# Performance work log

Measured on AMD Instinct MI355X. Metric: run time of the kernel, lower is better.

Reference implementation:

```python
import jax, jax.numpy as jnp
import numpy as np

H, P, G, NS, K = 8, 64, 64, 64, 3          # heads, dim_head, slice_num, d_state, d_conv
D_INNER = H * P                            # 512
CONV_DIM = D_INNER + 2 * NS                # 640
D_IN_PROJ = 2 * D_INNER + 2 * NS + 2 * H   # 1168


def setup_inputs() -> dict:
    key = jax.random.key(0)
    ks = jax.random.split(key, 10)
    dim, Bsz, N = 256, 4, 8192
    s = 0.02
    return {
        "x": jax.random.normal(ks[0], (Bsz, N, dim), jnp.float32),
        "W_fx": jax.random.normal(ks[1], (D_INNER, dim), jnp.float32) * s,
        "b_fx": jnp.zeros((D_INNER,), jnp.float32),
        "W_x": jax.random.normal(ks[2], (D_INNER, dim), jnp.float32) * s,
        "b_x": jnp.zeros((D_INNER,), jnp.float32),
        "W_slice": jax.random.normal(ks[3], (G, P), jnp.float32) * s,
        "b_slice": jnp.zeros((G,), jnp.float32),
        "temperature": jnp.full((1, H, 1, 1), 0.5, jnp.float32),
        "hy_in_w": jax.random.normal(ks[4], (D_IN_PROJ, D_INNER), jnp.float32) * s,
        "hy_conv_w": jax.random.normal(ks[5], (CONV_DIM, K), jnp.float32) * s,
        "hy_conv_b": jnp.zeros((CONV_DIM,), jnp.float32),
        "hy_dt_bias": jnp.log(jnp.expm1(jnp.full((H,), 0.01, jnp.float32))),
        "hy_A_log": jnp.log(jnp.linspace(1.0, 16.0, H)).astype(jnp.float32),
        "hy_D": jnp.ones((H,), jnp.float32),
        "hy_fcD_w": jax.random.normal(ks[6], (H, D_INNER), jnp.float32) * s,
        "hy_norm_w": jnp.ones((D_INNER,), jnp.float32),
        "hy_out_w": jax.random.normal(ks[7], (D_INNER, D_INNER), jnp.float32) * s,
        "out_w": jax.random.normal(ks[8], (dim, D_INNER), jnp.float32) * s,
        "out_b": jnp.zeros((dim,), jnp.float32),
    }


def _hydra(u, in_w, conv_w, conv_b, dt_bias, A_log, Dp, fcD_w, norm_w, out_w):
    # Bidirectional Mamba2-style selective scan (Hydra, non mem-eff path).
    Bt, L, _ = u.shape
    zxbcdt = u @ in_w.T                                   # (B, L, 1168)
    z = zxbcdt[..., :D_INNER]
    xBC = zxbcdt[..., D_INNER:D_INNER + CONV_DIM]
    dt = zxbcdt[..., -2 * H:]
    # fwd dts for fwd copies, time-flipped bwd dts stacked along batch
    dt = jnp.concatenate([dt[..., :H], jnp.flip(dt[..., H:], axis=1)], axis=0)
    dt = jax.nn.softplus(dt + dt_bias)                    # (2B, L, H)
    # depthwise causal conv, kernel K, left pad K-1 then silu
    xp = jnp.pad(xBC, ((0, 0), (K - 1, 0), (0, 0)))
    xBC = sum(xp[:, k:k + L, :] * conv_w[:, k] for k in range(K)) + conv_b
    xBC = jax.nn.silu(xBC)
    x = xBC[..., :D_INNER]
    Bm = xBC[..., D_INNER:D_INNER + NS]
    Cm = xBC[..., D_INNER + NS:]
    x_og = x
    x2 = jnp.concatenate([x, jnp.flip(x, 1)], 0).reshape(2 * Bt, L, H, P)
    B2 = jnp.concatenate([Bm, jnp.flip(Bm, 1)], 0)        # (2B, L, NS)
    C2 = jnp.concatenate([Cm, jnp.flip(Cm, 1)], 0)
    dA = jnp.exp(dt * (-jnp.exp(A_log)))                  # (2B, L, H)
    dBx = jnp.einsum('blh,bln,blhp->blhpn', dt, B2, x2)   # (2B, L, H, P, NS)

    def step(h, inp):
        dA_t, dBx_t, C_t = inp
        h = h * dA_t[:, :, None, None] + dBx_t
        return h, jnp.einsum('bhpn,bn->bhp', h, C_t)

    h0 = jnp.zeros((2 * Bt, H, P, NS), u.dtype)
    _, ys = jax.lax.scan(step, h0, (dA.transpose(1, 0, 2), dBx.transpose(1, 0, 2, 3, 4), C2.transpose(1, 0, 2)))
    y = ys.transpose(1, 0, 2, 3).reshape(2 * Bt, L, D_INNER)
    y_fw, y_bw = y[:Bt], jnp.flip(y[Bt:], 1)
    # quasiseparable: strictly-lower (shift fwd) + strictly-upper (shift bwd) + diagonal
    y = jnp.pad(y_fw[:, :-1], ((0, 0), (1, 0), (0, 0))) + jnp.pad(y_bw[:, 1:], ((0, 0), (0, 1), (0, 0)))
    y = y + x_og * jnp.repeat(x_og @ fcD_w.T + Dp, P, axis=-1)
    # gated RMSNorm (gate before norm), then out projection
    yg = y * jax.nn.silu(z)
    yg = yg * jax.lax.rsqrt(jnp.mean(jnp.square(yg), -1, keepdims=True) + 1e-5) * norm_w
    return yg @ out_w.T


def reference(x, W_fx, b_fx, W_x, b_x, W_slice, b_slice, temperature,
              hy_in_w, hy_conv_w, hy_conv_b, hy_dt_bias, hy_A_log, hy_D,
              hy_fcD_w, hy_norm_w, hy_out_w, out_w, out_b):
    B, N, _ = x.shape
    fx = (x @ W_fx.T + b_fx).reshape(B, N, H, P).transpose(0, 2, 1, 3)   # (B,H,N,P)
    xm = (x @ W_x.T + b_x).reshape(B, N, H, P).transpose(0, 2, 1, 3)
    temp = jnp.maximum(temperature, 1e-6)
    sw = jax.nn.softmax((xm @ W_slice.T + b_slice) / temp, axis=-1)      # (B,H,N,G)
    snorm = sw.sum(2)                                                     # (B,H,G)
    st = jnp.einsum('bhnc,bhng->bhgc', fx, sw) / (snorm + 1e-5)[..., None]
    st = st.transpose(0, 2, 1, 3).reshape(B, G, D_INNER)                  # (B,G,512)
    ot = _hydra(st, hy_in_w, hy_conv_w, hy_conv_b, hy_dt_bias, hy_A_log, hy_D,
                hy_fcD_w, hy_norm_w, hy_out_w)
    ot = ot.reshape(B, G, H, P).transpose(0, 2, 1, 3)                     # (B,H,G,P)
    out = jnp.einsum('bhgc,bhng->bhnc', ot, sw).transpose(0, 2, 1, 3).reshape(B, N, D_INNER)
    return out @ out_w.T + out_b
```

## Files before the change

kernel.cpp:

```cpp
#include <hip/hip_runtime.h>
#include <hip/hip_bf16.h>
#include <cstdint>
#include <cstddef>

#define Hh 8
#define DIN 512
#define CONVD 640
#define DPROJ 1168
#define NTOK 8192
#define DIM 256

typedef __attribute__((ext_vector_type(8))) short short8;
typedef __attribute__((ext_vector_type(4))) float f32x4;

static __device__ __forceinline__ float sigmoidf_(float x) { return 1.f / (1.f + expf(-x)); }
static __device__ __forceinline__ unsigned short f2b(float f) {
  __hip_bfloat16 h = __float2bfloat16(f);
  return *(unsigned short*)&h;
}
static __device__ __forceinline__ float b2f(unsigned short u) {
  union { unsigned int i; float f; } cv; cv.i = ((unsigned int)u) << 16; return cv.f;
}

__global__ __launch_bounds__(256) void k_cvt(
    const float* __restrict__ wfx, const float* __restrict__ wx, const float* __restrict__ outw,
    const float* __restrict__ inw, const float* __restrict__ how,
    const float* __restrict__ bfx, const float* __restrict__ bx,
    unsigned short* __restrict__ wcat, unsigned short* __restrict__ outwb,
    unsigned short* __restrict__ inwb, unsigned short* __restrict__ howb,
    float* __restrict__ bcat) {
  const int e = (blockIdx.x * 256 + threadIdx.x) * 4;
  if (e >= 1253376) {
    const int i = e - 1253376;
    float4 v;
    if (i < 512) v = *(const float4*)(bfx + i);
    else         v = *(const float4*)(bx + (i - 512));
    *(float4*)(bcat + i) = v;
    return;
  }
  const float* src; unsigned short* dst; int i;
  if (e < 131072)        { i = e;           src = wfx;  dst = wcat; }
  else if (e < 262144)   { i = e - 131072;  src = wx;   dst = wcat + 131072; }
  else if (e < 393216)   { i = e - 262144;  src = outw; dst = outwb; }
  else if (e < 991232)   { i = e - 393216;  src = inw;  dst = inwb; }
  else                   { i = e - 991232;  src = how;  dst = howb; }
  float4 v = *(const float4*)(src + i);
  ushort4 o;
  o.x = f2b(v.x); o.y = f2b(v.y); o.z = f2b(v.z); o.w = f2b(v.w);
  *(ushort4*)(dst + i) = o;
}

__global__ __launch_bounds__(256) void k_front(
    const float* __restrict__ x, const unsigned short* __restrict__ wcat,
    const float* __restrict__ bcat, const float* __restrict__ Wslice,
    const float* __restrict__ bslice, const float* __restrict__ temperature,
    unsigned short* __restrict__ cb, unsigned short* __restrict__ swb) {
  __shared__ unsigned short lds[17408];
  unsigned short* As = lds;
  unsigned short* Bs = lds + 8320;
  const int tid = threadIdx.x;
  const int m0 = blockIdx.x * 128;
  const int n0 = blockIdx.y * 128;
  const int w = tid >> 6, lane = tid & 63;
  const int l15 = lane & 15, kq = lane >> 4;
  const int wm = (w & 1) * 64, wn = (w >> 1) * 64;
  float bs[4];
#pragma unroll
  for (int j = 0; j < 4; ++j) bs[j] = bcat[n0 + wn + j * 16 + l15];
  f32x4 acc[4][4];
#pragma unroll
  for (int i = 0; i < 4; ++i)
#pragma unroll
    for (int j = 0; j < 4; ++j) acc[i][j] = (f32x4){0.f, 0.f, 0.f, 0.f};
  for (int kt = 0; kt < 256; kt += 64) {
#pragma unroll
    for (int i = 0; i < 4; ++i) {
      const int c = tid + 256 * i, m = c >> 3, kb = c & 7;
      const float* xs = &x[(size_t)(m0 + m) * 256 + kt + kb * 8];
      float4 v0 = *(const float4*)xs;
      float4 v1 = *(const float4*)(xs + 4);
      short8 av;
      av[0] = (short)f2b(v0.x); av[1] = (short)f2b(v0.y);
      av[2] = (short)f2b(v0.z); av[3] = (short)f2b(v0.w);
      av[4] = (short)f2b(v1.x); av[5] = (short)f2b(v1.y);
      av[6] = (short)f2b(v1.z); av[7] = (short)f2b(v1.w);
      *(short8*)&As[(kb * 130 + m) * 8] = av;
      *(short8*)&Bs[(kb * 130 + m) * 8] = *(const short8*)&wcat[(size_t)(n0 + m) * 256 + kt + kb * 8];
    }
    __syncthreads();
#pragma unroll
    for (int kw = 0; kw < 2; ++kw) {
      short8 af[4], bfr[4];
#pragma unroll
      for (int i = 0; i < 4; ++i) {
        af[i]  = *(const short8*)&As[((kw * 4 + kq) * 130 + wm + i * 16 + l15) * 8];
        bfr[i] = *(const short8*)&Bs[((kw * 4 + kq) * 130 + wn + i * 16 + l15) * 8];
      }
#pragma unroll
      for (int i = 0; i < 4; ++i)
#pragma unroll
        for (int j = 0; j < 4; ++j)
          acc[i][j] = __builtin_amdgcn_mfma_f32_16x16x32_bf16(af[i], bfr[j], acc[i][j], 0, 0, 0);
    }
    __syncthreads();
  }
  unsigned short* Cs = lds;
#pragma unroll
  for (int i = 0; i < 4; ++i)
#pragma unroll
    for (int j = 0; j < 4; ++j)
#pragma unroll
      for (int r = 0; r < 4; ++r) {
        const int m = wm + i * 16 + kq * 4 + r;
        const int n = wn + j * 16 + l15;
        Cs[m * 136 + n] = f2b(acc[i][j][r] + bs[j]);
      }
  __syncthreads();
  if (blockIdx.y < 4) {
#pragma unroll
    for (int it = 0; it < 8; ++it) {
      const int c = tid + 256 * it;
      const int m = c >> 4, seg = c & 15;
      *(short8*)&cb[(size_t)(m0 + m) * 512 + n0 + seg * 8] = *(const short8*)&Cs[m * 136 + seg * 8];
    }
    return;
  }
  const int h0 = (n0 - 512) >> 6;
  const int bidx = m0 >> 13, nb = m0 & (NTOK - 1);
  short8 sbfr[2][4];
#pragma unroll
  for (int kt = 0; kt < 2; ++kt)
#pragma unroll
    for (int j = 0; j < 4; ++j) {
      const float* wp = Wslice + (j * 16 + l15) * 64 + kt * 32 + kq * 8;
      short8 t;
#pragma unroll
      for (int u = 0; u < 8; ++u) t[u] = (short)f2b(wp[u]);
      sbfr[kt][j] = t;
    }
  float sbs[4];
#pragma unroll
  for (int j = 0; j < 4; ++j) sbs[j] = bslice[j * 16 + l15];
  f32x4 sacc[2][2][4];
#pragma unroll
  for (int hl = 0; hl < 2; ++hl)
#pragma unroll
    for (int i = 0; i < 2; ++i)
#pragma unroll
      for (int j = 0; j < 4; ++j) sacc[hl][i][j] = (f32x4){0.f, 0.f, 0.f, 0.f};
#pragma unroll
  for (int hl = 0; hl < 2; ++hl)
#pragma unroll
    for (int kt = 0; kt < 2; ++kt) {
      short8 af[2];
#pragma unroll
      for (int i = 0; i < 2; ++i)
        af[i] = *(const short8*)&Cs[(w * 32 + i * 16 + l15) * 136 + hl * 64 + kt * 32 + kq * 8];
#pragma unroll
      for (int i = 0; i < 2; ++i)
#pragma unroll
        for (int j = 0; j < 4; ++j)
          sacc[hl][i][j] = __builtin_amdgcn_mfma_f32_16x16x32_bf16(af[i], sbfr[kt][j], sacc[hl][i][j], 0, 0, 0);
    }
  __syncthreads();
#pragma unroll
  for (int hl = 0; hl < 2; ++hl) {
    const float invt = 1.f / fmaxf(temperature[h0 + hl], 1e-6f);
#pragma unroll
    for (int i = 0; i < 2; ++i)
#pragma unroll
      for (int r = 0; r < 4; ++r) {
        float v[4];
        float m = -1e30f;
#pragma unroll
        for (int j = 0; j < 4; ++j) { v[j] = (sacc[hl][i][j][r] + sbs[j]) * invt; m = fmaxf(m, v[j]); }
#pragma unroll
        for (int off = 8; off; off >>= 1) m = fmaxf(m, __shfl_xor(m, off));
        float s = 0.f;
#pragma unroll
        for (int j = 0; j < 4; ++j) { v[j] = expf(v[j] - m); s += v[j]; }
#pragma unroll
        for (int off = 8; off; off >>= 1) s += __shfl_xor(s, off);
        const float inv = 1.f / s;
        const int row = w * 32 + i * 16 + kq * 4 + r;
#pragma unroll
        for (int j = 0; j < 4; ++j) Cs[row * 136 + hl * 64 + j * 16 + l15] = f2b(v[j] * inv);
      }
  }
  __syncthreads();
#pragma unroll
  for (int it = 0; it < 8; ++it) {
    const int c = tid + 256 * it;
    const int head = c >> 10, row = (c >> 3) & 127, seg = c & 7;
    *(short8*)&swb[((size_t)(bidx * 8 + h0 + head) * NTOK + nb + row) * 64 + seg * 8] =
        *(const short8*)&Cs[row * 136 + head * 64 + seg * 8];
  }
}

__global__ __launch_bounds__(256) void k_st(
    const unsigned short* __restrict__ swb, const unsigned short* __restrict__ cb,
    float* __restrict__ st_raw, float* __restrict__ snorm) {
  __shared__ unsigned short swT[64][136];
  __shared__ unsigned short fxT[64][136];
  const int tid = threadIdx.x;
  const int bh = blockIdx.y;
  const int b = bh >> 3, h = bh & 7;
  const int nbase = blockIdx.x * 512;
  const int w = tid >> 6, lane = tid & 63;
  const int l15 = lane & 15, kq = lane >> 4;
  f32x4 acc[4];
#pragma unroll
  for (int i = 0; i < 4; ++i) acc[i] = (f32x4){0.f, 0.f, 0.f, 0.f};
  float sn = 0.f;
  for (int nc = 0; nc < 4; ++nc) {
    const int n0 = nbase + nc * 128;
#pragma unroll
    for (int i = 0; i < 4; ++i) {
      const int c = tid + 256 * i, n = c >> 3, gc = c & 7;
      short8 sv = *(const short8*)&swb[((size_t)bh * NTOK + n0 + n) * 64 + gc * 8];
      short8 fv = *(const short8*)&cb[((size_t)(b * NTOK) + n0 + n) * 512 + h * 64 + gc * 8];
#pragma unroll
      for (int u = 0; u < 8; ++u) {
        swT[gc * 8 + u][n] = (unsigned short)sv[u];
        fxT[gc * 8 + u][n] = (unsigned short)fv[u];
      }
    }
    __syncthreads();
    {
      const int g = tid & 63, q = tid >> 6;
#pragma unroll
      for (int nn = 0; nn < 32; ++nn) sn += b2f(swT[g][q * 32 + nn]);
    }
#pragma unroll
    for (int kw = 0; kw < 4; ++kw) {
      short8 bfr = *(const short8*)&fxT[w * 16 + l15][kw * 32 + kq * 8];
#pragma unroll
      for (int mi = 0; mi < 4; ++mi) {
        short8 af = *(const short8*)&swT[mi * 16 + l15][kw * 32 + kq * 8];
        acc[mi] = __builtin_amdgcn_mfma_f32_16x16x32_bf16(af, bfr, acc[mi], 0, 0, 0);
      }
    }
    __syncthreads();
  }
  float* stp = st_raw + (size_t)bh * 4096;
#pragma unroll
  for (int mi = 0; mi < 4; ++mi)
#pragma unroll
    for (int r = 0; r < 4; ++r)
      atomicAdd(&stp[(mi * 16 + kq * 4 + r) * 64 + w * 16 + l15], acc[mi][r]);
  atomicAdd(&snorm[bh * 64 + (tid & 63)], sn);
}

__global__ __launch_bounds__(256) void k_stnorm(
    const float* __restrict__ st_raw, const float* __restrict__ snorm,
    unsigned short* __restrict__ st2b) {
  const int idx = blockIdx.x * 256 + threadIdx.x;
  const int p = idx & 63, g = (idx >> 6) & 63, h = (idx >> 12) & 7, b = idx >> 15;
  const float v = st_raw[idx] / (snorm[(b * Hh + h) * 64 + g] + 1e-5f);
  st2b[(size_t)(b * 64 + g) * DIN + h * 64 + p] = f2b(v);
}

__global__ __launch_bounds__(256) void k_inproj(
    const unsigned short* __restrict__ st2b, const unsigned short* __restrict__ inwb,
    float* __restrict__ zx) {
  const int tid = threadIdx.x;
  const int m0 = blockIdx.x * 64;
  const int n0 = blockIdx.y * 64;
  const int w = tid >> 6, lane = tid & 63;
  const int l15 = lane & 15, kq = lane >> 4;
  f32x4 acc[4];
#pragma unroll
  for (int j = 0; j < 4; ++j) acc[j] = (f32x4){0.f, 0.f, 0.f, 0.f};
  const int arow = m0 + w * 16 + l15;
#pragma unroll
  for (int kc = 0; kc < 16; ++kc) {
    const short8 af = *(const short8*)&st2b[(size_t)arow * DIN + kc * 32 + kq * 8];
#pragma unroll
    for (int j = 0; j < 4; ++j) {
      int brow = n0 + j * 16 + l15;
      if (brow >= DPROJ) brow = 0;
      const short8 bfr = *(const short8*)&inwb[(size_t)brow * DIN + kc * 32 + kq * 8];
      acc[j] = __builtin_amdgcn_mfma_f32_16x16x32_bf16(af, bfr, acc[j], 0, 0, 0);
    }
  }
#pragma unroll
  for (int j = 0; j < 4; ++j)
#pragma unroll
    for (int r = 0; r < 4; ++r) {
      const int m = m0 + w * 16 + kq * 4 + r;
      const int c = n0 + j * 16 + l15;
      if (c < DPROJ) zx[(size_t)m * DPROJ + c] = acc[j][r];
    }
}

__global__ __launch_bounds__(256) void k_prep(
    const float* __restrict__ zx, const float* __restrict__ convw, const float* __restrict__ convb,
    const float* __restrict__ dtbias, const float* __restrict__ Alog,
    float* __restrict__ xbc, float* __restrict__ dt2, float* __restrict__ ldA2) {
  const int idx = blockIdx.x * 256 + threadIdx.x;
  const int NCONV = 4 * 64 * CONVD;
  if (idx < NCONV) {
    const int c = idx % CONVD;
    const int l = (idx / CONVD) & 63;
    const int b = idx / (CONVD * 64);
    float acc = convb[c];
#pragma unroll
    for (int k = 0; k < 3; ++k) {
      const int ls = l - 2 + k;
      if (ls >= 0) acc += zx[(size_t)(b * 64 + ls) * DPROJ + DIN + c] * convw[c * 3 + k];
    }
    xbc[idx] = acc * sigmoidf_(acc);
  } else if (idx < NCONV + 8 * 64 * 8) {
    const int j = idx - NCONV;
    const int h = j & 7, l = (j >> 3) & 63, bb = j >> 9;
    float raw;
    if (bb < 4) raw = zx[(size_t)(bb * 64 + l) * DPROJ + 1152 + h];
    else        raw = zx[(size_t)((bb - 4) * 64 + (63 - l)) * DPROJ + 1160 + h];
    const float d = raw + dtbias[h];
    const float sp = (d > 20.f) ? d : log1pf(expf(d));
    dt2[j] = sp;
    ldA2[j] = sp * -expf(Alog[h]);
  }
}

__global__ __launch_bounds__(256) void k_ssm(
    const float* __restrict__ xbc, const float* __restrict__ dt2, const float* __restrict__ ldA2,
    float* __restrict__ ys) {
  __shared__ unsigned short s_C[64][72];
  __shared__ unsigned short s_Bm[64][72];
  __shared__ unsigned short s_X[64][72];
  __shared__ unsigned short s_G[64][72];
  __shared__ float s_L[64];
  __shared__ float s_dt[64];
  const int blk = blockIdx.x;
  const int h = blk & 7, bb = blk >> 3;
  const int b = (bb < 4) ? bb : bb - 4;
  const bool rev = bb >= 4;
  const int tid = threadIdx.x;
  const int w = tid >> 6, lane = tid & 63;
  const int l15 = lane & 15, kq = lane >> 4;
  {
    const int l = tid >> 2, part = tid & 3;
    const int t = rev ? 63 - l : l;
    const float* src = xbc + (size_t)(b * 64 + l) * CONVD + DIN + part * 32;
#pragma unroll
    for (int u = 0; u < 32; u += 4) {
      float4 v = *(const float4*)(src + u);
      const int c = part * 32 + u;
      unsigned short* dst = (c < 64) ? &s_Bm[t][c] : &s_C[t][c - 64];
      dst[0] = f2b(v.x); dst[1] = f2b(v.y); dst[2] = f2b(v.z); dst[3] = f2b(v.w);
    }
    const float* xs = xbc + (size_t)(b * 64 + l) * CONVD + h * 64 + part * 16;
#pragma unroll
    for (int u = 0; u < 16; u += 4) {
      float4 v = *(const float4*)(xs + u);
      const int p = part * 16 + u;
      s_X[p + 0][t] = f2b(v.x); s_X[p + 1][t] = f2b(v.y);
      s_X[p + 2][t] = f2b(v.z); s_X[p + 3][t] = f2b(v.w);
    }
  }
  if (w == 0) {
    const float dtv = dt2[(bb * 64 + lane) * 8 + h];
    float ld = ldA2[(bb * 64 + lane) * 8 + h];
#pragma unroll
    for (int off = 1; off < 64; off <<= 1) {
      const float o = __shfl_up(ld, off);
      if (lane >= off) ld += o;
    }
    s_L[lane] = ld;
    s_dt[lane] = dtv;
  }
  __syncthreads();
  f32x4 accS[4];
#pragma unroll
  for (int i = 0; i < 4; ++i) accS[i] = (f32x4){0.f, 0.f, 0.f, 0.f};
#pragma unroll
  for (int kw = 0; kw < 2; ++kw) {
    const short8 bfr = *(const short8*)&s_Bm[w * 16 + l15][kw * 32 + kq * 8];
#pragma unroll
    for (int i = 0; i < 4; ++i) {
      const short8 af = *(const short8*)&s_C[i * 16 + l15][kw * 32 + kq * 8];
      accS[i] = __builtin_amdgcn_mfma_f32_16x16x32_bf16(af, bfr, accS[i], 0, 0, 0);
    }
  }
  const int s_idx = w * 16 + l15;
  const float Ls = s_L[s_idx];
  const float dts = s_dt[s_idx];
#pragma unroll
  for (int i = 0; i < 4; ++i)
#pragma unroll
    for (int r = 0; r < 4; ++r) {
      const int t = i * 16 + kq * 4 + r;
      const float g = (s_idx <= t) ? accS[i][r] * expf(s_L[t] - Ls) * dts : 0.f;
      s_G[t][s_idx] = f2b(g);
    }
  __syncthreads();
  f32x4 accY[4];
#pragma unroll
  for (int i = 0; i < 4; ++i) accY[i] = (f32x4){0.f, 0.f, 0.f, 0.f};
#pragma unroll
  for (int kw = 0; kw < 2; ++kw) {
    const short8 bfr = *(const short8*)&s_X[w * 16 + l15][kw * 32 + kq * 8];
#pragma unroll
    for (int i = 0; i < 4; ++i) {
      const short8 af = *(const short8*)&s_G[i * 16 + l15][kw * 32 + kq * 8];
      accY[i] = __builtin_amdgcn_mfma_f32_16x16x32_bf16(af, bfr, accY[i], 0, 0, 0);
    }
  }
#pragma unroll
  for (int i = 0; i < 4; ++i)
#pragma unroll
    for (int r = 0; r < 4; ++r) {
      const int t = i * 16 + kq * 4 + r;
      ys[(((size_t)(bb * 64 + t) * 8 + h) << 6) + w * 16 + l15] = accY[i][r];
    }
}

__global__ __launch_bounds__(256) void k_gate(
    const float* __restrict__ ys, const float* __restrict__ xbc, const float* __restrict__ zx,
    const float* __restrict__ fcdw, const float* __restrict__ Dp,
    const float* __restrict__ normw, unsigned short* __restrict__ ygb) {
  __shared__ float red[256][9];
  __shared__ float s_xfc[8];
  const int bl = blockIdx.x;
  const int b = bl >> 6, l = bl & 63;
  const int tid = threadIdx.x;
  const float xog0 = xbc[(size_t)bl * CONVD + tid];
  const float xog1 = xbc[(size_t)bl * CONVD + 256 + tid];
#pragma unroll
  for (int h = 0; h < 8; ++h)
    red[tid][h] = xog0 * fcdw[h * DIN + tid] + xog1 * fcdw[h * DIN + 256 + tid];
  __syncthreads();
  for (int s = 128; s > 0; s >>= 1) {
    if (tid < s) {
#pragma unroll
      for (int h = 0; h < 8; ++h) red[tid][h] += red[tid + s][h];
    }
    __syncthreads();
  }
  if (tid < 8) s_xfc[tid] = red[0][tid] + Dp[tid];
  __syncthreads();
  float ygv[2];
  float sumsq = 0.f;
#pragma unroll
  for (int ci = 0; ci < 2; ++ci) {
    const int c = tid + ci * 256;
    const int h = c >> 6, p = c & 63;
    float yv = 0.f;
    if (l >= 1)  yv += ys[(((size_t)(b * 64 + (l - 1)) * 8 + h) << 6) + p];
    if (l <= 62) yv += ys[(((size_t)((4 + b) * 64 + (62 - l)) * 8 + h) << 6) + p];
    const float xog = (ci == 0) ? xog0 : xog1;
    yv += xog * s_xfc[h];
    const float z = zx[(size_t)bl * DPROJ + c];
    const float g = yv * (z * sigmoidf_(z));
    ygv[ci] = g;
    sumsq += g * g;
  }
  red[tid][0] = sumsq;
  __syncthreads();
  for (int s = 128; s > 0; s >>= 1) {
    if (tid < s) red[tid][0] += red[tid + s][0];
    __syncthreads();
  }
  const float scale = 1.f / sqrtf(red[0][0] / 512.f + 1e-5f);
#pragma unroll
  for (int ci = 0; ci < 2; ++ci) {
    const int c = tid + ci * 256;
    ygb[(size_t)bl * DIN + c] = f2b(ygv[ci] * scale * normw[c]);
  }
}

__global__ __launch_bounds__(256) void k_oproj(
    const unsigned short* __restrict__ ygb, const unsigned short* __restrict__ howb,
    unsigned short* __restrict__ otT) {
  __shared__ unsigned short Cs[64][72];
  const int tid = threadIdx.x;
  const int b = blockIdx.x;
  const int h = blockIdx.y;
  const int m0 = b * 64, n0 = h * 64;
  const int w = tid >> 6, lane = tid & 63;
  const int l15 = lane & 15, kq = lane >> 4;
  f32x4 acc[4];
#pragma unroll
  for (int j = 0; j < 4; ++j) acc[j] = (f32x4){0.f, 0.f, 0.f, 0.f};
  const int arow = m0 + w * 16 + l15;
#pragma unroll
  for (int kc = 0; kc < 16; ++kc) {
    const short8 af = *(const short8*)&ygb[(size_t)arow * DIN + kc * 32 + kq * 8];
#pragma unroll
    for (int j = 0; j < 4; ++j) {
      const int brow = n0 + j * 16 + l15;
      const short8 bfr = *(const short8*)&howb[(size_t)brow * DIN + kc * 32 + kq * 8];
      acc[j] = __builtin_amdgcn_mfma_f32_16x16x32_bf16(af, bfr, acc[j], 0, 0, 0);
    }
  }
#pragma unroll
  for (int j = 0; j < 4; ++j)
#pragma unroll
    for (int r = 0; r < 4; ++r) {
      const int g = w * 16 + kq * 4 + r;
      const int p = j * 16 + l15;
      Cs[p][g] = f2b(acc[j][r]);
    }
  __syncthreads();
#pragma unroll
  for (int it = 0; it < 2; ++it) {
    const int c = tid + 256 * it;
    const int p = c >> 3, seg = c & 7;
    *(short8*)&otT[(((size_t)(b * 8 + h) * 64 + p) << 6) + seg * 8] = *(const short8*)&Cs[p][seg * 8];
  }
}

__global__ __launch_bounds__(256) void k_mixfinal(
    const unsigned short* __restrict__ swb, const unsigned short* __restrict__ otT,
    const unsigned short* __restrict__ outwb, const float* __restrict__ outb,
    float* __restrict__ out) {
  __shared__ unsigned short lm[33280];
  const int blk = blockIdx.x;
  const int b = blk >> 7;
  const int t0 = (blk & 127) * 64;
  const int tid = threadIdx.x;
  const int w = tid >> 6, lane = tid & 63;
  const int l15 = lane & 15, kq = lane >> 4;
#pragma unroll
  for (int hh = 0; hh < 2; ++hh) {
    const int h = w * 2 + hh;
    const int bh = b * 8 + h;
    f32x4 acc[4][4];
#pragma unroll
    for (int i = 0; i < 4; ++i)
#pragma unroll
      for (int j = 0; j < 4; ++j) acc[i][j] = (f32x4){0.f, 0.f, 0.f, 0.f};
#pragma unroll
    for (int kt = 0; kt < 2; ++kt) {
      short8 af[4], bfr[4];
#pragma unroll
      for (int i = 0; i < 4; ++i) {
        af[i]  = *(const short8*)&swb[((size_t)bh * NTOK + t0 + i * 16 + l15) * 64 + kt * 32 + kq * 8];
        bfr[i] = *(const short8*)&otT[(((size_t)bh * 64 + i * 16 + l15) << 6) + kt * 32 + kq * 8];
      }
#pragma unroll
      for (int i = 0; i < 4; ++i)
#pragma unroll
        for (int j = 0; j < 4; ++j)
          acc[i][j] = __builtin_amdgcn_mfma_f32_16x16x32_bf16(af[i], bfr[j], acc[i][j], 0, 0, 0);
    }
#pragma unroll
    for (int i = 0; i < 4; ++i)
#pragma unroll
      for (int j = 0; j < 4; ++j)
#pragma unroll
        for (int r = 0; r < 4; ++r)
          lm[(i * 16 + kq * 4 + r) * 520 + h * 64 + j * 16 + l15] = f2b(acc[i][j][r]);
  }
  __syncthreads();
  float ob[4];
#pragma unroll
  for (int j = 0; j < 4; ++j) ob[j] = outb[w * 64 + j * 16 + l15];
  f32x4 facc[4][4];
#pragma unroll
  for (int i = 0; i < 4; ++i)
#pragma unroll
    for (int j = 0; j < 4; ++j) facc[i][j] = (f32x4){0.f, 0.f, 0.f, 0.f};
#pragma unroll
  for (int kt = 0; kt < 16; ++kt) {
    short8 af[4], bfr[4];
#pragma unroll
    for (int i = 0; i < 4; ++i) {
      af[i]  = *(const short8*)&lm[(i * 16 + l15) * 520 + kt * 32 + kq * 8];
      bfr[i] = *(const short8*)&outwb[(size_t)(w * 64 + i * 16 + l15) * 512 + kt * 32 + kq * 8];
    }
#pragma unroll
    for (int i = 0; i < 4; ++i)
#pragma unroll
      for (int j = 0; j < 4; ++j)
        facc[i][j] = __builtin_amdgcn_mfma_f32_16x16x32_bf16(af[i], bfr[j], facc[i][j], 0, 0, 0);
  }
  __syncthreads();
  float* lf = (float*)lm;
#pragma unroll
  for (int i = 0; i < 4; ++i)
#pragma unroll
    for (int j = 0; j < 4; ++j)
#pragma unroll
      for (int r = 0; r < 4; ++r)
        lf[(i * 16 + kq * 4 + r) * 260 + w * 64 + j * 16 + l15] = facc[i][j][r] + ob[j];
  __syncthreads();
#pragma unroll
  for (int it = 0; it < 16; ++it) {
    const int c = tid + 256 * it;
    const int row = c >> 6, seg = c & 63;
    *(float4*)&out[((size_t)(b * NTOK + t0 + row)) * 256 + seg * 4] =
        *(const float4*)&lf[row * 260 + seg * 4];
  }
}

extern "C" void kernel_launch(void* const* d_in, const int* in_sizes, int n_in,
                              void* d_out, int out_size, void* d_ws, size_t ws_size,
                              hipStream_t stream) {
  const float* x      = (const float*)d_in[0];
  const float* Wfx    = (const float*)d_in[1];
  const float* bfx    = (const float*)d_in[2];
  const float* Wx     = (const float*)d_in[3];
  const float* bx     = (const float*)d_in[4];
  const float* Wslice = (const float*)d_in[5];
  const float* bslice = (const float*)d_in[6];
  const float* temp   = (const float*)d_in[7];
  const float* inw    = (const float*)d_in[8];
  const float* convw  = (const float*)d_in[9];
  const float* convb  = (const float*)d_in[10];
  const float* dtbias = (const float*)d_in[11];
  const float* Alog   = (const float*)d_in[12];
  const float* Dp     = (const float*)d_in[13];
  const float* fcdw   = (const float*)d_in[14];
  const float* normw  = (const float*)d_in[15];
  const float* how    = (const float*)d_in[16];
  const float* outw   = (const float*)d_in[17];
  const float* outb   = (const float*)d_in[18];

  unsigned short* us = (unsigned short*)d_ws;
  unsigned short* cb     = us;
  unsigned short* swb    = cb + 16777216;
  unsigned short* wcatb  = swb + 16777216;
  unsigned short* outwbf = wcatb + 262144;
  unsigned short* otTb   = outwbf + 131072;
  unsigned short* inwb   = otTb + 131072;
  unsigned short* howb   = inwb + 598016;
  unsigned short* st2b   = howb + 262144;
  unsigned short* ygbb   = st2b + 131072;
  float* fbase = (float*)(ygbb + 131072);
  float* bcat   = fbase;
  float* st_raw = bcat + 1024;
  float* snorm  = st_raw + 131072;
  float* zx     = snorm + 2048;
  float* xbc    = zx + 299008;
  float* dt2    = xbc + 163840;
  float* ldA2   = dt2 + 4096;
  float* ysb    = ldA2 + 4096;

  hipMemsetAsync(st_raw, 0, (131072 + 2048) * sizeof(float), stream);

  k_cvt     <<<dim3(1225),    256, 0, stream>>>(Wfx, Wx, outw, inw, how, bfx, bx,
                                                wcatb, outwbf, inwb, howb, bcat);
  k_front   <<<dim3(256, 8),  256, 0, stream>>>(x, wcatb, bcat, Wslice, bslice, temp, cb, swb);
  k_st      <<<dim3(16, 32),  256, 0, stream>>>(swb, cb, st_raw, snorm);
  k_stnorm  <<<dim3(512),     256, 0, stream>>>(st_raw, snorm, st2b);
  k_inproj  <<<dim3(4, 19),   256, 0, stream>>>(st2b, inwb, zx);
  k_prep    <<<dim3(656),     256, 0, stream>>>(zx, convw, convb, dtbias, Alog, xbc, dt2, ldA2);
  k_ssm     <<<dim3(64),      256, 0, stream>>>(xbc, dt2, ldA2, ysb);
  k_gate    <<<dim3(256),     256, 0, stream>>>(ysb, xbc, zx, fcdw, Dp, normw, ygbb);
  k_oproj   <<<dim3(4, 8),    256, 0, stream>>>(ygbb, howb, otTb);
  k_mixfinal<<<dim3(512),     256, 0, stream>>>(swb, otTb, outwbf, outb, (float*)d_out);
}
```

Baseline: 267.7 us.

## Emit transposed fx and slice-weight layouts from front GEMM, pre-convert x to bf16

The front GEMM now writes the fx projection and the softmax slice weights in a token-contiguous transposed layout (head*64+channel rows by token columns), alongside the existing slice-weight copy. The reduction kernel can then feed MFMA straight from global memory, with no LDS transpose and no barriers. The input x is converted to bf16 in a separate pre-pass inside the weight-convert kernel. In exchange it writes an extra full-size slice-weight copy and a bf16 copy of x, adding about 48 MB of global traffic, and k_front uses twice the shared memory.

```diff
diff --git a/kernel.cpp b/kernel.cpp
--- a/kernel.cpp
+++ b/kernel.cpp
@@ -23,15 +23,15 @@
 }
 
 __global__ __launch_bounds__(256) void k_cvt(
-    const float* __restrict__ wfx, const float* __restrict__ wx, const float* __restrict__ outw,
-    const float* __restrict__ inw, const float* __restrict__ how,
+    const float* __restrict__ x, const float* __restrict__ wfx, const float* __restrict__ wx,
+    const float* __restrict__ outw, const float* __restrict__ inw, const float* __restrict__ how,
     const float* __restrict__ bfx, const float* __restrict__ bx,
-    unsigned short* __restrict__ wcat, unsigned short* __restrict__ outwb,
-    unsigned short* __restrict__ inwb, unsigned short* __restrict__ howb,
-    float* __restrict__ bcat) {
+    unsigned short* __restrict__ xb, unsigned short* __restrict__ wcat,
+    unsigned short* __restrict__ outwb, unsigned short* __restrict__ inwb,
+    unsigned short* __restrict__ howb, float* __restrict__ bcat) {
   const int e = (blockIdx.x * 256 + threadIdx.x) * 4;
-  if (e >= 1253376) {
-    const int i = e - 1253376;
+  if (e >= 9641984) {
+    const int i = e - 9641984;
     float4 v;
     if (i < 512) v = *(const float4*)(bfx + i);
     else         v = *(const float4*)(bx + (i - 512));
@@ -39,11 +39,12 @@
     return;
   }
   const float* src; unsigned short* dst; int i;
-  if (e < 131072)        { i = e;           src = wfx;  dst = wcat; }
-  else if (e < 262144)   { i = e - 131072;  src = wx;   dst = wcat + 131072; }
-  else if (e < 393216)   { i = e - 262144;  src = outw; dst = outwb; }
-  else if (e < 991232)   { i = e - 393216;  src = inw;  dst = inwb; }
-  else                   { i = e - 991232;  src = how;  dst = howb; }
+  if (e < 8388608)       { i = e;           src = x;    dst = xb; }
+  else if (e < 8519680)  { i = e - 8388608; src = wfx;  dst = wcat; }
+  else if (e < 8650752)  { i = e - 8519680; src = wx;   dst = wcat + 131072; }
+  else if (e < 8781824)  { i = e - 8650752; src = outw; dst = outwb; }
+  else if (e < 9379840)  { i = e - 8781824; src = inw;  dst = inwb; }
+  else                   { i = e - 9379840; src = how;  dst = howb; }
   float4 v = *(const float4*)(src + i);
   ushort4 o;
   o.x = f2b(v.x); o.y = f2b(v.y); o.z = f2b(v.z); o.w = f2b(v.w);
@@ -51,11 +52,12 @@
 }
 
 __global__ __launch_bounds__(256) void k_front(
-    const float* __restrict__ x, const unsigned short* __restrict__ wcat,
+    const unsigned short* __restrict__ xb, const unsigned short* __restrict__ wcat,
     const float* __restrict__ bcat, const float* __restrict__ Wslice,
     const float* __restrict__ bslice, const float* __restrict__ temperature,
-    unsigned short* __restrict__ cb, unsigned short* __restrict__ swb) {
-  __shared__ unsigned short lds[17408];
+    unsigned short* __restrict__ cbT, unsigned short* __restrict__ swb,
+    unsigned short* __restrict__ swT) {
+  __shared__ unsigned short lds[34816];
   unsigned short* As = lds;
   unsigned short* Bs = lds + 8320;
   const int tid = threadIdx.x;
@@ -76,15 +78,7 @@
 #pragma unroll
     for (int i = 0; i < 4; ++i) {
       const int c = tid + 256 * i, m = c >> 3, kb = c & 7;
-      const float* xs = &x[(size_t)(m0 + m) * 256 + kt + kb * 8];
-      float4 v0 = *(const float4*)xs;
-      float4 v1 = *(const float4*)(xs + 4);
-      short8 av;
-      av[0] = (short)f2b(v0.x); av[1] = (short)f2b(v0.y);
-      av[2] = (short)f2b(v0.z); av[3] = (short)f2b(v0.w);
-      av[4] = (short)f2b(v1.x); av[5] = (short)f2b(v1.y);
-      av[6] = (short)f2b(v1.z); av[7] = (short)f2b(v1.w);
-      *(short8*)&As[(kb * 130 + m) * 8] = av;
+      *(short8*)&As[(kb * 130 + m) * 8] = *(const short8*)&xb[(size_t)(m0 + m) * 256 + kt + kb * 8];
       *(short8*)&Bs[(kb * 130 + m) * 8] = *(const short8*)&wcat[(size_t)(n0 + m) * 256 + kt + kb * 8];
     }
     __syncthreads();
@@ -104,7 +98,32 @@
     }
     __syncthreads();
   }
+  const int bidx = m0 >> 13, nb = m0 & (NTOK - 1);
+  if (blockIdx.y < 4) {
+    unsigned short* CsT = lds;
+#pragma unroll
+    for (int i = 0; i < 4; ++i)
+#pragma unroll
+      for (int j = 0; j < 4; ++j)
+#pragma unroll
+        for (int r = 0; r < 4; ++r) {
+          const int n = wm + i * 16 + kq * 4 + r;
+          const int pc = wn + j * 16 + l15;
+          CsT[pc * 136 + n] = f2b(acc[i][j][r] + bs[j]);
+        }
+    __syncthreads();
+    const int h0fx = blockIdx.y * 2;
+#pragma unroll
+    for (int it = 0; it < 8; ++it) {
+      const int c = tid + 256 * it;
+      const int pr = c >> 4, seg = c & 15;
+      const int row = (bidx * 8 + h0fx + (pr >> 6)) * 64 + (pr & 63);
+      *(short8*)&cbT[(size_t)row * NTOK + nb + seg * 8] = *(const short8*)&CsT[pr * 136 + seg * 8];
+    }
+    return;
+  }
   unsigned short* Cs = lds;
+  unsigned short* CsT2 = lds + 17408;
 #pragma unroll
   for (int i = 0; i < 4; ++i)
 #pragma unroll
@@ -116,17 +135,7 @@
         Cs[m * 136 + n] = f2b(acc[i][j][r] + bs[j]);
       }
   __syncthreads();
-  if (blockIdx.y < 4) {
-#pragma unroll
-    for (int it = 0; it < 8; ++it) {
-      const int c = tid + 256 * it;
-      const int m = c >> 4, seg = c & 15;
-      *(short8*)&cb[(size_t)(m0 + m) * 512 + n0 + seg * 8] = *(const short8*)&Cs[m * 136 + seg * 8];
-    }
-    return;
-  }
   const int h0 = (n0 - 512) >> 6;
-  const int bidx = m0 >> 13, nb = m0 & (NTOK - 1);
   short8 sbfr[2][4];
 #pragma unroll
   for (int kt = 0; kt < 2; ++kt)
@@ -184,7 +193,11 @@
         const float inv = 1.f / s;
         const int row = w * 32 + i * 16 + kq * 4 + r;
 #pragma unroll
-        for (int j = 0; j < 4; ++j) Cs[row * 136 + hl * 64 + j * 16 + l15] = f2b(v[j] * inv);
+        for (int j = 0; j < 4; ++j) {
+          const unsigned short sv = f2b(v[j] * inv);
+          Cs[row * 136 + hl * 64 + j * 16 + l15] = sv;
+          CsT2[(hl * 64 + j * 16 + l15) * 136 + row] = sv;
+        }
       }
   }
   __syncthreads();
@@ -195,52 +208,35 @@
     *(short8*)&swb[((size_t)(bidx * 8 + h0 + head) * NTOK + nb + row) * 64 + seg * 8] =
         *(const short8*)&Cs[row * 136 + head * 64 + seg * 8];
   }
+#pragma unroll
+  for (int it = 0; it < 8; ++it) {
+    const int c = tid + 256 * it;
+    const int gl = c >> 4, seg = c & 15;
+    const int grow = (bidx * 8 + h0 + (gl >> 6)) * 64 + (gl & 63);
+    *(short8*)&swT[(size_t)grow * NTOK + nb + seg * 8] = *(const short8*)&CsT2[gl * 136 + seg * 8];
+  }
 }
 
 __global__ __launch_bounds__(256) void k_st(
-    const unsigned short* __restrict__ swb, const unsigned short* __restrict__ cb,
+    const unsigned short* __restrict__ swT, const unsigned short* __restrict__ fxT,
     float* __restrict__ st_raw, float* __restrict__ snorm) {
-  __shared__ unsigned short swT[64][136];
-  __shared__ unsigned short fxT[64][136];
   const int tid = threadIdx.x;
   const int bh = blockIdx.y;
-  const int b = bh >> 3, h = bh & 7;
   const int nbase = blockIdx.x * 512;
   const int w = tid >> 6, lane = tid & 63;
   const int l15 = lane & 15, kq = lane >> 4;
   f32x4 acc[4];
 #pragma unroll
   for (int i = 0; i < 4; ++i) acc[i] = (f32x4){0.f, 0.f, 0.f, 0.f};
-  float sn = 0.f;
-  for (int nc = 0; nc < 4; ++nc) {
-    const int n0 = nbase + nc * 128;
-#pragma unroll
-    for (int i = 0; i < 4; ++i) {
-      const int c = tid + 256 * i, n = c >> 3, gc = c & 7;
-      short8 sv = *(const short8*)&swb[((size_t)bh * NTOK + n0 + n) * 64 + gc * 8];
-      short8 fv = *(const short8*)&cb[((size_t)(b * NTOK) + n0 + n) * 512 + h * 64 + gc * 8];
-#pragma unroll
-      for (int u = 0; u < 8; ++u) {
-        swT[gc * 8 + u][n] = (unsigned short)sv[u];
-        fxT[gc * 8 + u][n] = (unsigned short)fv[u];
-      }
-    }
-    __syncthreads();
-    {
-      const int g = tid & 63, q = tid >> 6;
-#pragma unroll
-      for (int nn = 0; nn < 32; ++nn) sn += b2f(swT[g][q * 32 + nn]);
-    }
-#pragma unroll
-    for (int kw = 0; kw < 4; ++kw) {
-      short8 bfr = *(const short8*)&fxT[w * 16 + l15][kw * 32 + kq * 8];
-#pragma unroll
-      for (int mi = 0; mi < 4; ++mi) {
-        short8 af = *(const short8*)&swT[mi * 16 + l15][kw * 32 + kq * 8];
-        acc[mi] = __builtin_amdgcn_mfma_f32_16x16x32_bf16(af, bfr, acc[mi], 0, 0, 0);
-      }
-    }
-    __syncthreads();
+#pragma unroll
+  for (int kc = 0; kc < 16; ++kc) {
+    const int noff = nbase + kc * 32 + kq * 8;
+    const short8 bfr = *(const short8*)&fxT[((size_t)bh * 64 + w * 16 + l15) * NTOK + noff];
+#pragma unroll
+    for (int mi = 0; mi < 4; ++mi) {
+      const short8 af = *(const short8*)&swT[((size_t)bh * 64 + mi * 16 + l15) * NTOK + noff];
+      acc[mi] = __builtin_amdgcn_mfma_f32_16x16x32_bf16(af, bfr, acc[mi], 0, 0, 0);
+    }
   }
   float* stp = st_raw + (size_t)bh * 4096;
 #pragma unroll
@@ -248,7 +244,18 @@
 #pragma unroll
     for (int r = 0; r < 4; ++r)
       atomicAdd(&stp[(mi * 16 + kq * 4 + r) * 64 + w * 16 + l15], acc[mi][r]);
-  atomicAdd(&snorm[bh * 64 + (tid & 63)], sn);
+  {
+    const int g = tid & 63, q = tid >> 6;
+    const unsigned short* sp = &swT[((size_t)bh * 64 + g) * NTOK + nbase + q * 128];
+    float sn = 0.f;
+#pragma unroll
+    for (int u = 0; u < 16; ++u) {
+      short8 sv = *(const short8*)&sp[u * 8];
+#pragma unroll
+      for (int e = 0; e < 8; ++e) sn += b2f((unsigned short)sv[e]);
+    }
+    atomicAdd(&snorm[bh * 64 + g], sn);
+  }
 }
 
 __global__ __launch_bounds__(256) void k_stnorm(
@@ -619,9 +626,11 @@
   const float* outb   = (const float*)d_in[18];
 
   unsigned short* us = (unsigned short*)d_ws;
-  unsigned short* cb     = us;
-  unsigned short* swb    = cb + 16777216;
-  unsigned short* wcatb  = swb + 16777216;
+  unsigned short* cbT    = us;
+  unsigned short* swb    = cbT + 16777216;
+  unsigned short* swTb   = swb + 16777216;
+  unsigned short* xbfb   = swTb + 16777216;
+  unsigned short* wcatb  = xbfb + 8388608;
   unsigned short* outwbf = wcatb + 262144;
   unsigned short* otTb   = outwbf + 131072;
   unsigned short* inwb   = otTb + 131072;
@@ -640,10 +649,11 @@
 
   hipMemsetAsync(st_raw, 0, (131072 + 2048) * sizeof(float), stream);
 
-  k_cvt     <<<dim3(1225),    256, 0, stream>>>(Wfx, Wx, outw, inw, how, bfx, bx,
-                                                wcatb, outwbf, inwb, howb, bcat);
-  k_front   <<<dim3(256, 8),  256, 0, stream>>>(x, wcatb, bcat, Wslice, bslice, temp, cb, swb);
-  k_st      <<<dim3(16, 32),  256, 0, stream>>>(swb, cb, st_raw, snorm);
+  k_cvt     <<<dim3(9417),    256, 0, stream>>>(x, Wfx, Wx, outw, inw, how, bfx, bx,
+                                                xbfb, wcatb, outwbf, inwb, howb, bcat);
+  k_front   <<<dim3(256, 8),  256, 0, stream>>>(xbfb, wcatb, bcat, Wslice, bslice, temp,
+                                                cbT, swb, swTb);
+  k_st      <<<dim3(16, 32),  256, 0, stream>>>(swTb, cbT, st_raw, snorm);
   k_stnorm  <<<dim3(512),     256, 0, stream>>>(st_raw, snorm, st2b);
   k_inproj  <<<dim3(4, 19),   256, 0, stream>>>(st2b, inwb, zx);
   k_prep    <<<dim3(656),     256, 0, stream>>>(zx, convw, convb, dtbias, Alog, xbc, dt2, ldA2);
```

Result: no change. 270.6 us (+1.1%).

## Pre-convert x to bf16 and fuse stnorm/prep into in-projection kernel

Applied to the files above, without the earlier changes.

Moves the fp32-to-bf16 conversion of x out of the front GEMM into the conversion kernel, so the GEMM loads bf16 directly, and adjusts the LDS padding stride. It also folds the st normalization into the in-projection A-load, and the conv/SiLU and dt softplus into the in-projection epilogue via a shared tile, which removes two launches and the zx round trip. zx now stores only the z part. The risk is the extra pass over x (write plus reread of a 16MB bf16 copy) in exchange for lighter GEMM loads.

```diff
diff --git a/kernel.cpp b/kernel.cpp
--- a/kernel.cpp
+++ b/kernel.cpp
@@ -23,15 +23,15 @@
 }
 
 __global__ __launch_bounds__(256) void k_cvt(
-    const float* __restrict__ wfx, const float* __restrict__ wx, const float* __restrict__ outw,
-    const float* __restrict__ inw, const float* __restrict__ how,
+    const float* __restrict__ x, const float* __restrict__ wfx, const float* __restrict__ wx,
+    const float* __restrict__ outw, const float* __restrict__ inw, const float* __restrict__ how,
     const float* __restrict__ bfx, const float* __restrict__ bx,
-    unsigned short* __restrict__ wcat, unsigned short* __restrict__ outwb,
-    unsigned short* __restrict__ inwb, unsigned short* __restrict__ howb,
-    float* __restrict__ bcat) {
+    unsigned short* __restrict__ xb, unsigned short* __restrict__ wcat,
+    unsigned short* __restrict__ outwb, unsigned short* __restrict__ inwb,
+    unsigned short* __restrict__ howb, float* __restrict__ bcat) {
   const int e = (blockIdx.x * 256 + threadIdx.x) * 4;
-  if (e >= 1253376) {
-    const int i = e - 1253376;
+  if (e >= 9641984) {
+    const int i = e - 9641984;
     float4 v;
     if (i < 512) v = *(const float4*)(bfx + i);
     else         v = *(const float4*)(bx + (i - 512));
@@ -39,11 +39,12 @@
     return;
   }
   const float* src; unsigned short* dst; int i;
-  if (e < 131072)        { i = e;           src = wfx;  dst = wcat; }
-  else if (e < 262144)   { i = e - 131072;  src = wx;   dst = wcat + 131072; }
-  else if (e < 393216)   { i = e - 262144;  src = outw; dst = outwb; }
-  else if (e < 991232)   { i = e - 393216;  src = inw;  dst = inwb; }
-  else                   { i = e - 991232;  src = how;  dst = howb; }
+  if (e < 8388608)       { i = e;           src = x;    dst = xb; }
+  else if (e < 8519680)  { i = e - 8388608; src = wfx;  dst = wcat; }
+  else if (e < 8650752)  { i = e - 8519680; src = wx;   dst = wcat + 131072; }
+  else if (e < 8781824)  { i = e - 8650752; src = outw; dst = outwb; }
+  else if (e < 9379840)  { i = e - 8781824; src = inw;  dst = inwb; }
+  else                   { i = e - 9379840; src = how;  dst = howb; }
   float4 v = *(const float4*)(src + i);
   ushort4 o;
   o.x = f2b(v.x); o.y = f2b(v.y); o.z = f2b(v.z); o.w = f2b(v.w);
@@ -51,13 +52,13 @@
 }
 
 __global__ __launch_bounds__(256) void k_front(
-    const float* __restrict__ x, const unsigned short* __restrict__ wcat,
+    const unsigned short* __restrict__ xb, const unsigned short* __restrict__ wcat,
     const float* __restrict__ bcat, const float* __restrict__ Wslice,
     const float* __restrict__ bslice, const float* __restrict__ temperature,
     unsigned short* __restrict__ cb, unsigned short* __restrict__ swb) {
   __shared__ unsigned short lds[17408];
   unsigned short* As = lds;
-  unsigned short* Bs = lds + 8320;
+  unsigned short* Bs = lds + 8384;
   const int tid = threadIdx.x;
   const int m0 = blockIdx.x * 128;
   const int n0 = blockIdx.y * 128;
@@ -76,16 +77,8 @@
 #pragma unroll
     for (int i = 0; i < 4; ++i) {
       const int c = tid + 256 * i, m = c >> 3, kb = c & 7;
-      const float* xs = &x[(size_t)(m0 + m) * 256 + kt + kb * 8];
-      float4 v0 = *(const float4*)xs;
-      float4 v1 = *(const float4*)(xs + 4);
-      short8 av;
-      av[0] = (short)f2b(v0.x); av[1] = (short)f2b(v0.y);
-      av[2] = (short)f2b(v0.z); av[3] = (short)f2b(v0.w);
-      av[4] = (short)f2b(v1.x); av[5] = (short)f2b(v1.y);
-      av[6] = (short)f2b(v1.z); av[7] = (short)f2b(v1.w);
-      *(short8*)&As[(kb * 130 + m) * 8] = av;
-      *(short8*)&Bs[(kb * 130 + m) * 8] = *(const short8*)&wcat[(size_t)(n0 + m) * 256 + kt + kb * 8];
+      *(short8*)&As[(kb * 131 + m) * 8] = *(const short8*)&xb[(size_t)(m0 + m) * 256 + kt + kb * 8];
+      *(short8*)&Bs[(kb * 131 + m) * 8] = *(const short8*)&wcat[(size_t)(n0 + m) * 256 + kt + kb * 8];
     }
     __syncthreads();
 #pragma unroll
@@ -93,8 +86,8 @@
       short8 af[4], bfr[4];
 #pragma unroll
       for (int i = 0; i < 4; ++i) {
-        af[i]  = *(const short8*)&As[((kw * 4 + kq) * 130 + wm + i * 16 + l15) * 8];
-        bfr[i] = *(const short8*)&Bs[((kw * 4 + kq) * 130 + wn + i * 16 + l15) * 8];
+        af[i]  = *(const short8*)&As[((kw * 4 + kq) * 131 + wm + i * 16 + l15) * 8];
+        bfr[i] = *(const short8*)&Bs[((kw * 4 + kq) * 131 + wn + i * 16 + l15) * 8];
       }
 #pragma unroll
       for (int i = 0; i < 4; ++i)
@@ -116,6 +109,7 @@
         Cs[m * 136 + n] = f2b(acc[i][j][r] + bs[j]);
       }
   __syncthreads();
+  const int bidx = m0 >> 13, nb = m0 & (NTOK - 1);
   if (blockIdx.y < 4) {
 #pragma unroll
     for (int it = 0; it < 8; ++it) {
@@ -126,7 +120,6 @@
     return;
   }
   const int h0 = (n0 - 512) >> 6;
-  const int bidx = m0 >> 13, nb = m0 & (NTOK - 1);
   short8 sbfr[2][4];
 #pragma unroll
   for (int kt = 0; kt < 2; ++kt)
@@ -251,30 +244,33 @@
   atomicAdd(&snorm[bh * 64 + (tid & 63)], sn);
 }
 
-__global__ __launch_bounds__(256) void k_stnorm(
+__global__ __launch_bounds__(256) void k_inproj(
     const float* __restrict__ st_raw, const float* __restrict__ snorm,
-    unsigned short* __restrict__ st2b) {
-  const int idx = blockIdx.x * 256 + threadIdx.x;
-  const int p = idx & 63, g = (idx >> 6) & 63, h = (idx >> 12) & 7, b = idx >> 15;
-  const float v = st_raw[idx] / (snorm[(b * Hh + h) * 64 + g] + 1e-5f);
-  st2b[(size_t)(b * 64 + g) * DIN + h * 64 + p] = f2b(v);
-}
-
-__global__ __launch_bounds__(256) void k_inproj(
-    const unsigned short* __restrict__ st2b, const unsigned short* __restrict__ inwb,
-    float* __restrict__ zx) {
+    const unsigned short* __restrict__ inwb,
+    const float* __restrict__ convw, const float* __restrict__ convb,
+    const float* __restrict__ dtbias, const float* __restrict__ Alog,
+    float* __restrict__ zx, float* __restrict__ xbc,
+    float* __restrict__ dt2, float* __restrict__ ldA2) {
+  __shared__ float Zs[64][68];
   const int tid = threadIdx.x;
-  const int m0 = blockIdx.x * 64;
-  const int n0 = blockIdx.y * 64;
+  const int b = blockIdx.x;
+  const int y = blockIdx.y;
+  const int n0 = y * 64;
   const int w = tid >> 6, lane = tid & 63;
   const int l15 = lane & 15, kq = lane >> 4;
   f32x4 acc[4];
 #pragma unroll
   for (int j = 0; j < 4; ++j) acc[j] = (f32x4){0.f, 0.f, 0.f, 0.f};
-  const int arow = m0 + w * 16 + l15;
+  const int g = w * 16 + l15;
 #pragma unroll
   for (int kc = 0; kc < 16; ++kc) {
-    const short8 af = *(const short8*)&st2b[(size_t)arow * DIN + kc * 32 + kq * 8];
+    const int col0 = kc * 32 + kq * 8;
+    const int h = col0 >> 6, p0 = col0 & 63;
+    const float rcp = 1.f / (snorm[(b * 8 + h) * 64 + g] + 1e-5f);
+    const float* sp = &st_raw[(((size_t)(b * 8 + h) * 64 + g) << 6) + p0];
+    short8 af;
+#pragma unroll
+    for (int u = 0; u < 8; ++u) af[u] = (short)f2b(sp[u] * rcp);
 #pragma unroll
     for (int j = 0; j < 4; ++j) {
       int brow = n0 + j * 16 + l15;
@@ -286,40 +282,43 @@
 #pragma unroll
   for (int j = 0; j < 4; ++j)
 #pragma unroll
-    for (int r = 0; r < 4; ++r) {
-      const int m = m0 + w * 16 + kq * 4 + r;
-      const int c = n0 + j * 16 + l15;
-      if (c < DPROJ) zx[(size_t)m * DPROJ + c] = acc[j][r];
-    }
-}
-
-__global__ __launch_bounds__(256) void k_prep(
-    const float* __restrict__ zx, const float* __restrict__ convw, const float* __restrict__ convb,
-    const float* __restrict__ dtbias, const float* __restrict__ Alog,
-    float* __restrict__ xbc, float* __restrict__ dt2, float* __restrict__ ldA2) {
-  const int idx = blockIdx.x * 256 + threadIdx.x;
-  const int NCONV = 4 * 64 * CONVD;
-  if (idx < NCONV) {
-    const int c = idx % CONVD;
-    const int l = (idx / CONVD) & 63;
-    const int b = idx / (CONVD * 64);
-    float acc = convb[c];
-#pragma unroll
-    for (int k = 0; k < 3; ++k) {
-      const int ls = l - 2 + k;
-      if (ls >= 0) acc += zx[(size_t)(b * 64 + ls) * DPROJ + DIN + c] * convw[c * 3 + k];
-    }
-    xbc[idx] = acc * sigmoidf_(acc);
-  } else if (idx < NCONV + 8 * 64 * 8) {
-    const int j = idx - NCONV;
-    const int h = j & 7, l = (j >> 3) & 63, bb = j >> 9;
-    float raw;
-    if (bb < 4) raw = zx[(size_t)(bb * 64 + l) * DPROJ + 1152 + h];
-    else        raw = zx[(size_t)((bb - 4) * 64 + (63 - l)) * DPROJ + 1160 + h];
-    const float d = raw + dtbias[h];
-    const float sp = (d > 20.f) ? d : log1pf(expf(d));
-    dt2[j] = sp;
-    ldA2[j] = sp * -expf(Alog[h]);
+    for (int r = 0; r < 4; ++r)
+      Zs[w * 16 + kq * 4 + r][j * 16 + l15] = acc[j][r];
+  __syncthreads();
+  if (y < 8) {
+#pragma unroll
+    for (int it = 0; it < 4; ++it) {
+      const int idx = tid + 256 * it;
+      const int row = idx >> 4, f4 = idx & 15;
+      *(float4*)&zx[(size_t)(b * 64 + row) * 512 + n0 + f4 * 4] = *(const float4*)&Zs[row][f4 * 4];
+    }
+  } else if (y < 18) {
+    const int c0 = n0 - 512;
+#pragma unroll
+    for (int it = 0; it < 16; ++it) {
+      const int idx = tid + 256 * it;
+      const int l = idx >> 6, cl = idx & 63;
+      const int c = c0 + cl;
+      float a = convb[c];
+#pragma unroll
+      for (int k = 0; k < 3; ++k) {
+        const int ls = l - 2 + k;
+        if (ls >= 0) a += Zs[ls][cl] * convw[c * 3 + k];
+      }
+      xbc[(size_t)(b * 64 + l) * CONVD + c] = a * sigmoidf_(a);
+    }
+  } else {
+#pragma unroll
+    for (int it = 0; it < 4; ++it) {
+      const int idx = tid + 256 * it;
+      const int dir = idx >> 9, l = (idx >> 3) & 63, h = idx & 7;
+      const float raw = dir ? Zs[63 - l][8 + h] : Zs[l][h];
+      const float d = raw + dtbias[h];
+      const float sp = (d > 20.f) ? d : log1pf(expf(d));
+      const int jj = (((dir * 4 + b) * 64) + l) * 8 + h;
+      dt2[jj] = sp;
+      ldA2[jj] = sp * -expf(Alog[h]);
+    }
   }
 }
 
@@ -451,7 +450,7 @@
     if (l <= 62) yv += ys[(((size_t)((4 + b) * 64 + (62 - l)) * 8 + h) << 6) + p];
     const float xog = (ci == 0) ? xog0 : xog1;
     yv += xog * s_xfc[h];
-    const float z = zx[(size_t)bl * DPROJ + c];
+    const float z = zx[(size_t)bl * 512 + c];
     const float g = yv * (z * sigmoidf_(z));
     ygv[ci] = g;
     sumsq += g * g;
@@ -621,32 +620,31 @@
   unsigned short* us = (unsigned short*)d_ws;
   unsigned short* cb     = us;
   unsigned short* swb    = cb + 16777216;
-  unsigned short* wcatb  = swb + 16777216;
+  unsigned short* xbfb   = swb + 16777216;
+  unsigned short* wcatb  = xbfb + 8388608;
   unsigned short* outwbf = wcatb + 262144;
   unsigned short* otTb   = outwbf + 131072;
   unsigned short* inwb   = otTb + 131072;
   unsigned short* howb   = inwb + 598016;
-  unsigned short* st2b   = howb + 262144;
-  unsigned short* ygbb   = st2b + 131072;
+  unsigned short* ygbb   = howb + 262144;
   float* fbase = (float*)(ygbb + 131072);
   float* bcat   = fbase;
   float* st_raw = bcat + 1024;
   float* snorm  = st_raw + 131072;
   float* zx     = snorm + 2048;
-  float* xbc    = zx + 299008;
+  float* xbc    = zx + 131072;
   float* dt2    = xbc + 163840;
   float* ldA2   = dt2 + 4096;
   float* ysb    = ldA2 + 4096;
 
   hipMemsetAsync(st_raw, 0, (131072 + 2048) * sizeof(float), stream);
 
-  k_cvt     <<<dim3(1225),    256, 0, stream>>>(Wfx, Wx, outw, inw, how, bfx, bx,
-                                                wcatb, outwbf, inwb, howb, bcat);
-  k_front   <<<dim3(256, 8),  256, 0, stream>>>(x, wcatb, bcat, Wslice, bslice, temp, cb, swb);
+  k_cvt     <<<dim3(9417),    256, 0, stream>>>(x, Wfx, Wx, outw, inw, how, bfx, bx,
+                                                xbfb, wcatb, outwbf, inwb, howb, bcat);
+  k_front   <<<dim3(256, 8),  256, 0, stream>>>(xbfb, wcatb, bcat, Wslice, bslice, temp, cb, swb);
   k_st      <<<dim3(16, 32),  256, 0, stream>>>(swb, cb, st_raw, snorm);
-  k_stnorm  <<<dim3(512),     256, 0, stream>>>(st_raw, snorm, st2b);
-  k_inproj  <<<dim3(4, 19),   256, 0, stream>>>(st2b, inwb, zx);
-  k_prep    <<<dim3(656),     256, 0, stream>>>(zx, convw, convb, dtbias, Alog, xbc, dt2, ldA2);
+  k_inproj  <<<dim3(4, 19),   256, 0, stream>>>(st_raw, snorm, inwb, convw, convb, dtbias, Alog,
+                                                zx, xbc, dt2, ldA2);
   k_ssm     <<<dim3(64),      256, 0, stream>>>(xbc, dt2, ldA2, ysb);
   k_gate    <<<dim3(256),     256, 0, stream>>>(ysb, xbc, zx, fcdw, Dp, normw, ygbb);
   k_oproj   <<<dim3(4, 8),    256, 0, stream>>>(ygbb, howb, otTb);
```

Result: slower. 281.1 us (+5.0%).
